# Optimization experiments

Measured on AMD Instinct MI355X. Metric: run time of the kernel, lower is better.

The kernel has to match this reference:

```python
import jax, jax.numpy as jnp
import numpy as np

PC_RANGE = (-51.2, -51.2, -5.0, 51.2, 51.2, 3.0)
NUM_HEADS = 8
K_TOKENS = 512
DS = 4  # bev_downsample


def _ln(x, w, b):
    m = x.mean(-1, keepdims=True)
    v = ((x - m) ** 2).mean(-1, keepdims=True)
    return (x - m) * jax.lax.rsqrt(v + 1e-5) * w + b


def _mlp(x, w1, b1, w2, b2):
    return jnp.maximum(x @ w1.T + b1, 0.0) @ w2.T + b2


def setup_inputs() -> dict:
    key = jax.random.key(0)
    ks = jax.random.split(key, 16)
    B, N, Dq, Dkv, H, W = 2, 1220, 512, 256, 512, 512
    s = 0.02
    rn = lambda k, shp: jax.random.normal(k, shp, jnp.float32) * s
    inp = {
        'instance_feature': jax.random.normal(ks[0], (B, N, Dq), jnp.float32),
        'pts_feats': jax.random.normal(ks[1], (B, Dkv, H, W), jnp.float32),
        'anchor': jax.random.normal(ks[2], (B, N, 11), jnp.float32) * 20.0,
        # cross-attention (kdim=vdim=256, embed_dim=512)
        'qw': rn(ks[3], (Dq, Dq)), 'qb': jnp.zeros((Dq,), jnp.float32),
        'kw': rn(ks[4], (Dq, Dkv)), 'kb': jnp.zeros((Dq,), jnp.float32),
        'vw': rn(ks[5], (Dq, Dkv)), 'vb': jnp.zeros((Dq,), jnp.float32),
        'aow': rn(ks[6], (Dq, Dq)), 'aob': jnp.zeros((Dq,), jnp.float32),
        # layer norms
        'qn_w': jnp.ones((Dq,), jnp.float32), 'qn_b': jnp.zeros((Dq,), jnp.float32),
        'tn_w': jnp.ones((Dkv,), jnp.float32), 'tn_b': jnp.zeros((Dkv,), jnp.float32),
        'on_w': jnp.ones((Dq,), jnp.float32), 'on_b': jnp.zeros((Dq,), jnp.float32),
        # out_proj
        'opw': rn(ks[7], (Dq, Dq)), 'opb': jnp.zeros((Dq,), jnp.float32),
        # bev_pos_mlp: Linear(2,256) -> ReLU -> Linear(256,256)
        'bp_w1': rn(ks[8], (Dkv, 2)), 'bp_b1': jnp.zeros((Dkv,), jnp.float32),
        'bp_w2': rn(ks[9], (Dkv, Dkv)), 'bp_b2': jnp.zeros((Dkv,), jnp.float32),
        # anchor_pos_mlp: Linear(2,512) -> ReLU -> Linear(512,512)
        'ap_w1': rn(ks[10], (Dq, 2)), 'ap_b1': jnp.zeros((Dq,), jnp.float32),
        'ap_w2': rn(ks[11], (Dq, Dq)), 'ap_b2': jnp.zeros((Dq,), jnp.float32),
        # gate: Linear(512,512) -> ReLU -> Linear(512,512) -> Sigmoid, bias init -2.0
        'g_w1': rn(ks[12], (Dq, Dq)), 'g_b1': jnp.zeros((Dq,), jnp.float32),
        'g_w2': rn(ks[13], (Dq, Dq)), 'g_b2': jnp.full((Dq,), -2.0, jnp.float32),
    }
    return inp


def reference(instance_feature, pts_feats, anchor,
              qw, qb, kw, kb, vw, vb, aow, aob,
              qn_w, qn_b, tn_w, tn_b, on_w, on_b,
              opw, opb,
              bp_w1, bp_b1, bp_w2, bp_b2,
              ap_w1, ap_b1, ap_w2, ap_b2,
              g_w1, g_b1, g_w2, g_b2):
    B, C, H0, W0 = pts_feats.shape
    # avg_pool2d(kernel=stride=DS)
    H, W = H0 // DS, W0 // DS
    bev = pts_feats.reshape(B, C, H, DS, W, DS).mean(axis=(3, 5))  # [B,C,H,W]
    # topk token selection by mean squared activation
    score = (bev ** 2).mean(axis=1).reshape(B, H * W)
    K = min(K_TOKENS, H * W)
    _, idx = jax.lax.top_k(score, K)  # [B,K], sorted descending
    tokens = bev.reshape(B, C, H * W).transpose(0, 2, 1)  # [B,HW,C]
    lidar_tokens = jnp.take_along_axis(tokens, idx[..., None], axis=1)  # [B,K,C]
    ys = idx // W
    xs = idx % W
    token_pos = jnp.stack([(xs.astype(jnp.float32) + 0.5) / W,
                           (ys.astype(jnp.float32) + 0.5) / H], axis=-1)  # [B,K,2]
    lidar_tokens = lidar_tokens + _mlp(token_pos, bp_w1, bp_b1, bp_w2, bp_b2)
    # anchor positional prior (anchor detached in original)
    xr = (anchor[..., 0] - PC_RANGE[0]) / (PC_RANGE[3] - PC_RANGE[0])
    yr = (anchor[..., 1] - PC_RANGE[1]) / (PC_RANGE[4] - PC_RANGE[1])
    xy = jnp.clip(jnp.stack([xr, yr], axis=-1), 0.0, 1.0)
    query_input = instance_feature + _mlp(xy, ap_w1, ap_b1, ap_w2, ap_b2)
    query = _ln(query_input, qn_w, qn_b)
    kv = _ln(lidar_tokens, tn_w, tn_b)
    # multihead cross-attention (dropout off / eval mode)
    Dq = query.shape[-1]
    hd = Dq // NUM_HEADS
    q = (query @ qw.T + qb).reshape(B, -1, NUM_HEADS, hd)  # [B,N,h,d]
    k = (kv @ kw.T + kb).reshape(B, K, NUM_HEADS, hd)      # [B,K,h,d]
    v = (kv @ vw.T + vb).reshape(B, K, NUM_HEADS, hd)
    scale = 1.0 / jnp.sqrt(jnp.float32(hd))
    att = jax.nn.softmax(jnp.einsum('bnhd,bkhd->bhnk', q, k) * scale, axis=-1)
    ctx = jnp.einsum('bhnk,bkhd->bnhd', att, v).reshape(B, -1, Dq)
    ctx = ctx @ aow.T + aob  # MHA out_proj
    lidar_context = _ln(ctx @ opw.T + opb, on_w, on_b)
    gate = jax.nn.sigmoid(_mlp(query_input, g_w1, g_b1, g_w2, g_b2))
    return instance_feature + gate * lidar_context
```

## Files before the change

### kernel.cpp

```cpp
#include <hip/hip_runtime.h>
#include <hip/hip_bf16.h>
#include <math.h>

constexpr int BB  = 2;
constexpr int NN  = 1220;
constexpr int DKV = 256;
constexpr int H0  = 512, W0 = 512;
constexpr int HH  = 128, WW = 128;
constexpr int HW  = HH * WW;
constexpr int KT  = 512;
constexpr int MR  = BB * NN;
constexpr int MPAD = 2496;

typedef __attribute__((ext_vector_type(8)))  short bf16x8;
typedef __attribute__((ext_vector_type(4)))  float f32x4;
typedef __attribute__((ext_vector_type(16))) float f32x16;

constexpr size_t B_BEV   = 0;
constexpr size_t B_SCORE = 67108864;
constexpr size_t B_IDX   = 67239936;
constexpr size_t B_WBF   = 67244032;
constexpr size_t B_KV    = 70914048;
constexpr size_t B_KG    = 71438336;
constexpr size_t B_VG    = 72486912;
constexpr size_t B_VT    = 73535488;
constexpr size_t B_H1    = 74584064;
constexpr size_t B_QI32  = 77139968;
constexpr size_t B_QI16  = 82251776;
constexpr size_t B_QUERY = 84807680;
constexpr size_t B_QG    = 87363584;
constexpr size_t B_CTX   = 89919488;
constexpr size_t B_AO    = 92475392;
constexpr size_t B_OPO   = 95031296;
constexpr size_t B_LC    = 100143104;
constexpr size_t B_G1    = 105254912;
constexpr size_t WS_NEED = 107810816;

constexpr size_t WO_QW = 0, WO_KW = 262144, WO_VW = 393216, WO_AOW = 524288,
                 WO_OPW = 786432, WO_APW2 = 1048576, WO_GW1 = 1310720, WO_GW2 = 1572864;

__device__ __forceinline__ void gload_lds16(void* lds, const void* g) {
  __builtin_amdgcn_global_load_lds((const __attribute__((address_space(1))) unsigned int*)g,
                                   (__attribute__((address_space(3))) unsigned int*)lds, 16, 0, 0);
}

__device__ __forceinline__ unsigned cvt_pk_bf16(float a, float b) {
  unsigned r;
  asm("v_cvt_pk_bf16_f32 %0, %1, %2" : "=v"(r) : "v"(a), "v"(b));
  return r;
}

__global__ __launch_bounds__(256) void wconv_kernel(
    const float* __restrict__ qw, const float* __restrict__ kw,
    const float* __restrict__ vw, const float* __restrict__ aow,
    const float* __restrict__ opw, const float* __restrict__ apw2,
    const float* __restrict__ gw1, const float* __restrict__ gw2,
    __hip_bfloat16* __restrict__ dst) {
  int i = blockIdx.x * 256 + threadIdx.x;
  const float* src; int off;
  if (i < 262144)       { src = qw;   off = 0; }
  else if (i < 393216)  { src = kw;   off = 262144; }
  else if (i < 524288)  { src = vw;   off = 393216; }
  else if (i < 786432)  { src = aow;  off = 524288; }
  else if (i < 1048576) { src = opw;  off = 786432; }
  else if (i < 1310720) { src = apw2; off = 1048576; }
  else if (i < 1572864) { src = gw1;  off = 1310720; }
  else                  { src = gw2;  off = 1572864; }
  dst[i] = __float2bfloat16(src[i - off]);
}

__global__ __launch_bounds__(256) void pool_kernel(const float* __restrict__ pts,
                                                   float* __restrict__ bev) {
  int o = blockIdx.x * 256 + threadIdx.x;
  int w  = o & (WW - 1);
  int h  = (o >> 7) & (HH - 1);
  int bc = o >> 14;
  const float* p = pts + ((bc * H0) + h * 4) * W0 + w * 4;
  float s = 0.f;
#pragma unroll
  for (int r = 0; r < 4; ++r) {
    float4 v = *(const float4*)(p + r * W0);
    s += v.x + v.y + v.z + v.w;
  }
  bev[o] = s * (1.f / 16.f);
}

__global__ __launch_bounds__(256) void score_kernel(const float* __restrict__ bev,
                                                    float* __restrict__ score) {
  int t = blockIdx.x * 256 + threadIdx.x;
  int b = t >> 14, p = t & (HW - 1);
  const float* base = bev + (size_t)(b * DKV) * HW + p;
  float acc = 0.f;
  for (int c = 0; c < DKV; ++c) {
    float v = base[c * HW];
    acc += v * v;
  }
  score[t] = acc * (1.f / DKV);
}

__global__ __launch_bounds__(1024) void topk_kernel(const float* __restrict__ score,
                                                    int* __restrict__ idx) {
  int b = blockIdx.x;
  const float* s = score + b * HW;
  __shared__ int hist[16][256];
  __shared__ int htot[256];
  __shared__ int sh_digit, sh_need, sh_cnt;
  int tid = threadIdx.x;
  int wv = tid >> 6;
  unsigned prefix = 0;
  int need = KT;
  for (int pass = 0; pass < 4; ++pass) {
    int shift = 24 - pass * 8;
    if (tid < 256) {
#pragma unroll
      for (int w = 0; w < 16; ++w) hist[w][tid] = 0;
    }
    __syncthreads();
    for (int p = tid; p < HW; p += 1024) {
      unsigned u = __float_as_uint(s[p]);
      bool match = (pass == 0) || ((u >> (shift + 8)) == prefix);
      if (match) atomicAdd(&hist[wv][(u >> shift) & 255], 1);
    }
    __syncthreads();
    if (tid < 256) {
      int t = 0;
#pragma unroll
      for (int w = 0; w < 16; ++w) t += hist[w][tid];
      htot[tid] = t;
    }
    __syncthreads();
    for (int off = 1; off < 256; off <<= 1) {
      int v = 0;
      if (tid < 256) v = htot[tid] + ((tid + off < 256) ? htot[tid + off] : 0);
      __syncthreads();
      if (tid < 256) htot[tid] = v;
      __syncthreads();
    }
    if (tid < 256) {
      int sfx = htot[tid], sfx1 = (tid < 255) ? htot[tid + 1] : 0;
      if (sfx >= need && sfx1 < need) { sh_digit = tid; sh_need = need - sfx1; }
    }
    __syncthreads();
    prefix = (prefix << 8) | (unsigned)sh_digit;
    need = sh_need;
    __syncthreads();
  }
  unsigned T = prefix;
  int r = need;
  if (tid == 0) sh_cnt = 0;
  __syncthreads();
  for (int p = tid; p < HW; p += 1024) {
    if (__float_as_uint(s[p]) > T) {
      int pos = atomicAdd(&sh_cnt, 1);
      idx[b * KT + pos] = p;
    }
  }
  __syncthreads();
  int base = sh_cnt;
  if (tid < 64) {
    int taken = 0;
    for (int c0 = 0; c0 < HW && taken < r; c0 += 64) {
      int p = c0 + tid;
      bool eq = (__float_as_uint(s[p]) == T);
      unsigned long long m = __ballot(eq);
      int rank = __popcll(m & ((1ull << tid) - 1ull));
      if (eq && (taken + rank) < r) idx[b * KT + base + taken + rank] = p;
      taken += __popcll(m);
    }
  }
}

__global__ __launch_bounds__(256) void token_kernel(const float* __restrict__ bev,
    const int* __restrict__ idx,
    const float* __restrict__ bw1, const float* __restrict__ bb1,
    const float* __restrict__ bw2, const float* __restrict__ bb2,
    const float* __restrict__ tw, const float* __restrict__ tb,
    __hip_bfloat16* __restrict__ kv) {
  int blk = blockIdx.x;
  int b = blk >> 9;
  int c = threadIdx.x;
  int p = idx[blk];
  float val = bev[(size_t)(b * DKV + c) * HW + p];
  float px = ((p & (WW - 1)) + 0.5f) * (1.f / WW);
  float py = ((p >> 7) + 0.5f) * (1.f / HH);
  __shared__ float h1[DKV];
  __shared__ float red[DKV];
  h1[c] = fmaxf(bw1[c * 2] * px + bw1[c * 2 + 1] * py + bb1[c], 0.f);
  __syncthreads();
  float o = bb2[c];
  const float4* w4 = (const float4*)(bw2 + c * DKV);
#pragma unroll 4
  for (int j = 0; j < DKV / 4; ++j) {
    float4 w = w4[j];
    o += w.x * h1[j * 4] + w.y * h1[j * 4 + 1] + w.z * h1[j * 4 + 2] + w.w * h1[j * 4 + 3];
  }
  float tokv = val + o;
  red[c] = tokv; __syncthreads();
  for (int st = 128; st > 0; st >>= 1) { if (c < st) red[c] += red[c + st]; __syncthreads(); }
  float mean = red[0] * (1.f / DKV);
  __syncthreads();
  float d = tokv - mean;
  red[c] = d * d; __syncthreads();
  for (int st = 128; st > 0; st >>= 1) { if (c < st) red[c] += red[c + st]; __syncthreads(); }
  float inv = rsqrtf(red[0] * (1.f / DKV) + 1e-5f);
  kv[(size_t)blk * DKV + c] = __float2bfloat16(d * inv * tw[c] + tb[c]);
}

__global__ __launch_bounds__(256) void ap1_kernel(const float* __restrict__ anchor,
    const float* __restrict__ w1, const float* __restrict__ b1,
    __hip_bfloat16* __restrict__ h) {
  int g = blockIdx.x * 256 + threadIdx.x;
  int row = g >> 9, col = g & 511;
  float ax = anchor[row * 11 + 0];
  float ay = anchor[row * 11 + 1];
  float xr = fminf(fmaxf((ax + 51.2f) * (1.f / 102.4f), 0.f), 1.f);
  float yr = fminf(fmaxf((ay + 51.2f) * (1.f / 102.4f), 0.f), 1.f);
  h[g] = __float2bfloat16(fmaxf(w1[col * 2] * xr + w1[col * 2 + 1] * yr + b1[col], 0.f));
}

template <int EPI>
__global__ __launch_bounds__(256) void mgemm(
    const short* __restrict__ A, const short* __restrict__ W,
    const float* __restrict__ bias, const float* __restrict__ aux1,
    const float* __restrict__ aux2, void* __restrict__ o1, void* __restrict__ o2,
    int M, int Nd, int Kd) {
  __shared__ short As[64 * 64];
  __shared__ short Bs[64 * 64];
  const int tid = threadIdx.x;
  const int wave = tid >> 6, lane = tid & 63;
  const int m0 = blockIdx.y * 64, n0 = blockIdx.x * 64;
  const int wr = wave >> 1, wc = wave & 1;
  f32x4 acc[2][2];
#pragma unroll
  for (int i = 0; i < 2; ++i)
#pragma unroll
    for (int j = 0; j < 2; ++j) acc[i][j] = (f32x4){0.f, 0.f, 0.f, 0.f};

  const int srow = lane >> 3;
  const int sslot = lane & 7;
  for (int k0 = 0; k0 < Kd; k0 += 64) {
#pragma unroll
    for (int half = 0; half < 2; ++half) {
      int r = wave * 16 + half * 8 + srow;
      int ss = sslot ^ (r & 7);
      gload_lds16(As + (wave * 16 + half * 8) * 64,
                  A + (size_t)(m0 + r) * Kd + k0 + ss * 8);
      gload_lds16(Bs + (wave * 16 + half * 8) * 64,
                  W + (size_t)(n0 + r) * Kd + k0 + ss * 8);
    }
    __syncthreads();
#pragma unroll
    for (int ks = 0; ks < 2; ++ks) {
      bf16x8 af[2], bf[2];
#pragma unroll
      for (int mf = 0; mf < 2; ++mf) {
        int r = wr * 32 + mf * 16 + (lane & 15);
        int slot = (ks * 4 + (lane >> 4)) ^ (r & 7);
        af[mf] = *(const bf16x8*)(As + r * 64 + slot * 8);
      }
#pragma unroll
      for (int nf = 0; nf < 2; ++nf) {
        int r = wc * 32 + nf * 16 + (lane & 15);
        int slot = (ks * 4 + (lane >> 4)) ^ (r & 7);
        bf[nf] = *(const bf16x8*)(Bs + r * 64 + slot * 8);
      }
#pragma unroll
      for (int mf = 0; mf < 2; ++mf)
#pragma unroll
        for (int nf = 0; nf < 2; ++nf)
          acc[mf][nf] = __builtin_amdgcn_mfma_f32_16x16x32_bf16(af[mf], bf[nf], acc[mf][nf], 0, 0, 0);
    }
    __syncthreads();
  }
#pragma unroll
  for (int mf = 0; mf < 2; ++mf)
#pragma unroll
    for (int nf = 0; nf < 2; ++nf) {
      int col = n0 + wc * 32 + nf * 16 + (lane & 15);
      float bv = bias[col];
#pragma unroll
      for (int i = 0; i < 4; ++i) {
        int row = m0 + wr * 32 + mf * 16 + (lane >> 4) * 4 + i;
        if (row < M) {
          float v = acc[mf][nf][i] + bv;
          size_t off = (size_t)row * Nd + col;
          if (EPI == 0) ((__hip_bfloat16*)o1)[off] = __float2bfloat16(v);
          else if (EPI == 1) {
            v += aux1[off];
            ((float*)o1)[off] = v;
            ((__hip_bfloat16*)o2)[off] = __float2bfloat16(v);
          } else if (EPI == 2) ((__hip_bfloat16*)o1)[off] = __float2bfloat16(fmaxf(v, 0.f));
          else if (EPI == 3) ((__hip_bfloat16*)o1)[off] = __float2bfloat16(v * 0.125f);
          else if (EPI == 4) ((float*)o1)[off] = v;
          else if (EPI == 5) {
            float g = 1.f / (1.f + __expf(-v));
            ((float*)o1)[off] = aux1[off] + g * aux2[off];
          }
        }
      }
    }
}

template <int OUT_BF16>
__global__ __launch_bounds__(256) void ln512_kernel(const float* __restrict__ in,
    void* __restrict__ outp, const float* __restrict__ w, const float* __restrict__ bb) {
  int row = blockIdx.x, tid = threadIdx.x;
  float x0 = in[(size_t)row * 512 + tid];
  float x1 = in[(size_t)row * 512 + 256 + tid];
  __shared__ float rs[256], rq[256];
  rs[tid] = x0 + x1;
  rq[tid] = x0 * x0 + x1 * x1;
  __syncthreads();
  for (int o = 128; o > 0; o >>= 1) {
    if (tid < o) { rs[tid] += rs[tid + o]; rq[tid] += rq[tid + o]; }
    __syncthreads();
  }
  float mean = rs[0] * (1.f / 512.f);
  float var = rq[0] * (1.f / 512.f) - mean * mean;
  float inv = rsqrtf(var + 1e-5f);
  float y0 = (x0 - mean) * inv * w[tid] + bb[tid];
  float y1 = (x1 - mean) * inv * w[256 + tid] + bb[256 + tid];
  if (OUT_BF16) {
    ((__hip_bfloat16*)outp)[(size_t)row * 512 + tid] = __float2bfloat16(y0);
    ((__hip_bfloat16*)outp)[(size_t)row * 512 + 256 + tid] = __float2bfloat16(y1);
  } else {
    ((float*)outp)[(size_t)row * 512 + tid] = y0;
    ((float*)outp)[(size_t)row * 512 + 256 + tid] = y1;
  }
}

__global__ __launch_bounds__(256) void vtrans_kernel(const short* __restrict__ V,
                                                     short* __restrict__ Vt) {
  __shared__ short tile[128][72];
  int tc = blockIdx.x, h = blockIdx.y, b = blockIdx.z;
  int tid = threadIdx.x;
#pragma unroll
  for (int it = 0; it < 8; ++it) {
    int e = it * 256 + tid;
    int r = e >> 4, c = (e & 15) * 4;
    *(short4*)&tile[r][c] =
        *(const short4*)(V + ((size_t)(b * 512 + tc * 128 + r)) * 512 + h * 64 + c);
  }
  __syncthreads();
#pragma unroll
  for (int it = 0; it < 8; ++it) {
    int e = it * 256 + tid;
    int d = e >> 5, t4 = (e & 31) * 4;
    short4 v;
    v.x = tile[t4 + 0][d]; v.y = tile[t4 + 1][d];
    v.z = tile[t4 + 2][d]; v.w = tile[t4 + 3][d];
    *(short4*)(Vt + (((size_t)(b * 8 + h)) * 64 + d) * 512 + tc * 128 + t4) = v;
  }
}

__global__ __launch_bounds__(256) void attn_kernel(
    const short* __restrict__ Qg, const short* __restrict__ Kg,
    const short* __restrict__ Vt, __hip_bfloat16* __restrict__ ctx) {
  int tid = threadIdx.x;
  int wid = blockIdx.x * 4 + (tid >> 6);
  int lane = tid & 63;
  int l31 = lane & 31, lhi = lane >> 5;
  int qc = wid % 39;
  int bh = wid / 39;
  int h = bh & 7, b = bh >> 3;
  int n = qc * 32 + l31;
  size_t qrow = (size_t)b * NN + n;
  const short* qp = Qg + qrow * 512 + h * 64 + lhi * 8;
  bf16x8 qf0 = *(const bf16x8*)(qp);
  bf16x8 qf1 = *(const bf16x8*)(qp + 16);
  bf16x8 qf2 = *(const bf16x8*)(qp + 32);
  bf16x8 qf3 = *(const bf16x8*)(qp + 48);
  f32x16 ot0 = {}, ot1 = {};
  float m_run = -1e30f, lsum = 0.f;
  const short* kbase = Kg + ((size_t)(b * KT) + l31) * 512 + h * 64 + lhi * 8;
  const short* vbase = Vt + (((size_t)(b * 8 + h)) * 64 + l31) * 512 + lhi * 8;
  for (int tc = 0; tc < 16; ++tc) {
    const short* kp = kbase + (size_t)(tc * 32) * 512;
    bf16x8 kf0 = *(const bf16x8*)(kp);
    bf16x8 kf1 = *(const bf16x8*)(kp + 16);
    bf16x8 kf2 = *(const bf16x8*)(kp + 32);
    bf16x8 kf3 = *(const bf16x8*)(kp + 48);
    const short* vp = vbase + tc * 32;
    bf16x8 v00 = *(const bf16x8*)(vp);
    bf16x8 v01 = *(const bf16x8*)(vp + 16);
    bf16x8 v10 = *(const bf16x8*)(vp + 32 * 512);
    bf16x8 v11 = *(const bf16x8*)(vp + 32 * 512 + 16);
    f32x16 s = {};
    s = __builtin_amdgcn_mfma_f32_32x32x16_bf16(kf0, qf0, s, 0, 0, 0);
    s = __builtin_amdgcn_mfma_f32_32x32x16_bf16(kf1, qf1, s, 0, 0, 0);
    s = __builtin_amdgcn_mfma_f32_32x32x16_bf16(kf2, qf2, s, 0, 0, 0);
    s = __builtin_amdgcn_mfma_f32_32x32x16_bf16(kf3, qf3, s, 0, 0, 0);
    float pmax = s[0];
#pragma unroll
    for (int i = 1; i < 16; ++i) pmax = fmaxf(pmax, s[i]);
    pmax = fmaxf(pmax, __shfl_xor(pmax, 32));
    float m_new = fmaxf(m_run, pmax);
    float corr = __expf(m_run - m_new);
    m_run = m_new;
    lsum *= corr;
#pragma unroll
    for (int i = 0; i < 16; ++i) { ot0[i] *= corr; ot1[i] *= corr; }
    float p[16];
    float psum = 0.f;
#pragma unroll
    for (int i = 0; i < 16; ++i) { p[i] = __expf(s[i] - m_new); psum += p[i]; }
    lsum += psum;
    unsigned w0 = cvt_pk_bf16(p[0], p[1]),  w1 = cvt_pk_bf16(p[2], p[3]);
    unsigned w2 = cvt_pk_bf16(p[4], p[5]),  w3 = cvt_pk_bf16(p[6], p[7]);
    unsigned w4 = cvt_pk_bf16(p[8], p[9]),  w5 = cvt_pk_bf16(p[10], p[11]);
    unsigned w6 = cvt_pk_bf16(p[12], p[13]), w7 = cvt_pk_bf16(p[14], p[15]);
    unsigned sw0 = (unsigned)__shfl_xor((int)w0, 32), sw1 = (unsigned)__shfl_xor((int)w1, 32);
    unsigned sw2 = (unsigned)__shfl_xor((int)w2, 32), sw3 = (unsigned)__shfl_xor((int)w3, 32);
    unsigned sw4 = (unsigned)__shfl_xor((int)w4, 32), sw5 = (unsigned)__shfl_xor((int)w5, 32);
    unsigned sw6 = (unsigned)__shfl_xor((int)w6, 32), sw7 = (unsigned)__shfl_xor((int)w7, 32);
    union UU { unsigned u[4]; bf16x8 v; };
    UU ub0, ub1;
    ub0.u[0] = lhi ? sw2 : w0; ub0.u[1] = lhi ? sw3 : w1;
    ub0.u[2] = lhi ? w2 : sw0; ub0.u[3] = lhi ? w3 : sw1;
    ub1.u[0] = lhi ? sw6 : w4; ub1.u[1] = lhi ? sw7 : w5;
    ub1.u[2] = lhi ? w6 : sw4; ub1.u[3] = lhi ? w7 : sw5;
    ot0 = __builtin_amdgcn_mfma_f32_32x32x16_bf16(v00, ub0.v, ot0, 0, 0, 0);
    ot0 = __builtin_amdgcn_mfma_f32_32x32x16_bf16(v01, ub1.v, ot0, 0, 0, 0);
    ot1 = __builtin_amdgcn_mfma_f32_32x32x16_bf16(v10, ub0.v, ot1, 0, 0, 0);
    ot1 = __builtin_amdgcn_mfma_f32_32x32x16_bf16(v11, ub1.v, ot1, 0, 0, 0);
  }
  lsum += __shfl_xor(lsum, 32);
  float inv = 1.f / lsum;
  if (n < NN) {
    __hip_bfloat16* cp = ctx + qrow * 512 + h * 64;
#pragma unroll
    for (int r = 0; r < 16; ++r) {
      int d = (r & 3) + 8 * (r >> 2) + 4 * lhi;
      cp[d]      = __float2bfloat16(ot0[r] * inv);
      cp[32 + d] = __float2bfloat16(ot1[r] * inv);
    }
  }
}

extern "C" void kernel_launch(void* const* d_in, const int* in_sizes, int n_in,
                              void* d_out, int out_size, void* d_ws, size_t ws_size,
                              hipStream_t stream) {
  const float* inst   = (const float*)d_in[0];
  const float* pts    = (const float*)d_in[1];
  const float* anchor = (const float*)d_in[2];
  const float* qw  = (const float*)d_in[3];
  const float* qb  = (const float*)d_in[4];
  const float* kw  = (const float*)d_in[5];
  const float* kb  = (const float*)d_in[6];
  const float* vw  = (const float*)d_in[7];
  const float* vb  = (const float*)d_in[8];
  const float* aow = (const float*)d_in[9];
  const float* aob = (const float*)d_in[10];
  const float* qnw = (const float*)d_in[11];
  const float* qnb = (const float*)d_in[12];
  const float* tnw = (const float*)d_in[13];
  const float* tnb = (const float*)d_in[14];
  const float* onw = (const float*)d_in[15];
  const float* onb = (const float*)d_in[16];
  const float* opw = (const float*)d_in[17];
  const float* opb = (const float*)d_in[18];
  const float* bpw1 = (const float*)d_in[19];
  const float* bpb1 = (const float*)d_in[20];
  const float* bpw2 = (const float*)d_in[21];
  const float* bpb2 = (const float*)d_in[22];
  const float* apw1 = (const float*)d_in[23];
  const float* apb1 = (const float*)d_in[24];
  const float* apw2 = (const float*)d_in[25];
  const float* apb2 = (const float*)d_in[26];
  const float* gw1 = (const float*)d_in[27];
  const float* gb1 = (const float*)d_in[28];
  const float* gw2 = (const float*)d_in[29];
  const float* gb2 = (const float*)d_in[30];
  float* out = (float*)d_out;

  if (ws_size < WS_NEED) return;
  char* ws = (char*)d_ws;
  float* bev   = (float*)(ws + B_BEV);
  float* score = (float*)(ws + B_SCORE);
  int*   idx   = (int*)(ws + B_IDX);
  short* wbf   = (short*)(ws + B_WBF);
  __hip_bfloat16* kvb = (__hip_bfloat16*)(ws + B_KV);
  short* Kgb  = (short*)(ws + B_KG);
  short* Vgb  = (short*)(ws + B_VG);
  short* Vtb  = (short*)(ws + B_VT);
  short* h1b  = (short*)(ws + B_H1);
  float* qi32 = (float*)(ws + B_QI32);
  short* qi16 = (short*)(ws + B_QI16);
  short* qryb = (short*)(ws + B_QUERY);
  short* Qgb  = (short*)(ws + B_QG);
  short* ctxb = (short*)(ws + B_CTX);
  short* aobuf = (short*)(ws + B_AO);
  float* opo  = (float*)(ws + B_OPO);
  float* lc   = (float*)(ws + B_LC);
  short* g1b  = (short*)(ws + B_G1);

  wconv_kernel<<<7168, 256, 0, stream>>>(qw, kw, vw, aow, opw, apw2, gw1, gw2,
                                         (__hip_bfloat16*)wbf);
  pool_kernel<<<BB * DKV * HW / 256, 256, 0, stream>>>(pts, bev);
  score_kernel<<<BB * HW / 256, 256, 0, stream>>>(bev, score);
  topk_kernel<<<BB, 1024, 0, stream>>>(score, idx);
  token_kernel<<<BB * KT, 256, 0, stream>>>(bev, idx, bpw1, bpb1, bpw2, bpb2, tnw, tnb, kvb);
  mgemm<0><<<dim3(8, 16), 256, 0, stream>>>((const short*)kvb, wbf + WO_KW, kb,
                                            nullptr, nullptr, Kgb, nullptr, 1024, 512, 256);
  mgemm<0><<<dim3(8, 16), 256, 0, stream>>>((const short*)kvb, wbf + WO_VW, vb,
                                            nullptr, nullptr, Vgb, nullptr, 1024, 512, 256);
  vtrans_kernel<<<dim3(4, 8, BB), 256, 0, stream>>>(Vgb, Vtb);
  ap1_kernel<<<MR * 512 / 256, 256, 0, stream>>>(anchor, apw1, apb1, (__hip_bfloat16*)h1b);
  mgemm<1><<<dim3(8, 39), 256, 0, stream>>>(h1b, wbf + WO_APW2, apb2, inst, nullptr,
                                            qi32, qi16, MR, 512, 512);
  ln512_kernel<1><<<MR, 256, 0, stream>>>(qi32, qryb, qnw, qnb);
  mgemm<3><<<dim3(8, 39), 256, 0, stream>>>(qryb, wbf + WO_QW, qb, nullptr, nullptr,
                                            Qgb, nullptr, MR, 512, 512);
  attn_kernel<<<156, 256, 0, stream>>>(Qgb, Kgb, Vtb, (__hip_bfloat16*)ctxb);
  mgemm<0><<<dim3(8, 39), 256, 0, stream>>>(ctxb, wbf + WO_AOW, aob, nullptr, nullptr,
                                            aobuf, nullptr, MR, 512, 512);
  mgemm<4><<<dim3(8, 39), 256, 0, stream>>>(aobuf, wbf + WO_OPW, opb, nullptr, nullptr,
                                            opo, nullptr, MR, 512, 512);
  ln512_kernel<0><<<MR, 256, 0, stream>>>(opo, lc, onw, onb);
  mgemm<2><<<dim3(8, 39), 256, 0, stream>>>(qi16, wbf + WO_GW1, gb1, nullptr, nullptr,
                                            g1b, nullptr, MR, 512, 512);
  mgemm<5><<<dim3(8, 39), 256, 0, stream>>>(g1b, wbf + WO_GW2, gb2, inst, lc,
                                            out, nullptr, MR, 512, 512);
}
```

Baseline: 357.1 us.

## Use 128x64 double-buffered LDS tiles in mgemm and shrink workspace layout

Result: slower. 381.3 us (+6.8%).

```diff
diff --git a/kernel.cpp b/kernel.cpp
--- a/kernel.cpp
+++ b/kernel.cpp
@@ -10,31 +10,31 @@
 constexpr int HW  = HH * WW;
 constexpr int KT  = 512;
 constexpr int MR  = BB * NN;
-constexpr int MPAD = 2496;
+constexpr int MPAD = 2560;
 
 typedef __attribute__((ext_vector_type(8)))  short bf16x8;
 typedef __attribute__((ext_vector_type(4)))  float f32x4;
 typedef __attribute__((ext_vector_type(16))) float f32x16;
 
 constexpr size_t B_BEV   = 0;
-constexpr size_t B_SCORE = 67108864;
-constexpr size_t B_IDX   = 67239936;
-constexpr size_t B_WBF   = 67244032;
-constexpr size_t B_KV    = 70914048;
-constexpr size_t B_KG    = 71438336;
-constexpr size_t B_VG    = 72486912;
-constexpr size_t B_VT    = 73535488;
-constexpr size_t B_H1    = 74584064;
-constexpr size_t B_QI32  = 77139968;
-constexpr size_t B_QI16  = 82251776;
-constexpr size_t B_QUERY = 84807680;
-constexpr size_t B_QG    = 87363584;
-constexpr size_t B_CTX   = 89919488;
-constexpr size_t B_AO    = 92475392;
-constexpr size_t B_OPO   = 95031296;
-constexpr size_t B_LC    = 100143104;
-constexpr size_t B_G1    = 105254912;
-constexpr size_t WS_NEED = 107810816;
+constexpr size_t B_SCORE = 33554432;
+constexpr size_t B_IDX   = 33685504;
+constexpr size_t B_WBF   = 33689600;
+constexpr size_t B_KV    = 37359616;
+constexpr size_t B_KG    = 37883904;
+constexpr size_t B_VG    = 38932480;
+constexpr size_t B_VT    = 39981056;
+constexpr size_t B_H1    = 41029632;
+constexpr size_t B_QI32  = 43651072;
+constexpr size_t B_QI16  = 48893952;
+constexpr size_t B_QUERY = 51515392;
+constexpr size_t B_QG    = 54136832;
+constexpr size_t B_CTX   = 56758272;
+constexpr size_t B_AO    = 59379712;
+constexpr size_t B_OPO   = 62001152;
+constexpr size_t B_LC    = 67244032;
+constexpr size_t B_G1    = 72486912;
+constexpr size_t WS_NEED = 75112448;
 
 constexpr size_t WO_QW = 0, WO_KW = 262144, WO_VW = 393216, WO_AOW = 524288,
                  WO_OPW = 786432, WO_APW2 = 1048576, WO_GW1 = 1310720, WO_GW2 = 1572864;
@@ -180,7 +180,7 @@
   int b = blk >> 9;
   int c = threadIdx.x;
   int p = idx[blk];
-  float val = bev[(size_t)(b * DKV + c) * HW + p];
+  float val = bev[((size_t)(b * DKV + c) << 14) + p];
   float px = ((p & (WW - 1)) + 0.5f) * (1.f / WW);
   float py = ((p >> 7) + 0.5f) * (1.f / HH);
   __shared__ float h1[DKV];
@@ -224,63 +224,76 @@
     const float* __restrict__ bias, const float* __restrict__ aux1,
     const float* __restrict__ aux2, void* __restrict__ o1, void* __restrict__ o2,
     int M, int Nd, int Kd) {
-  __shared__ short As[64 * 64];
-  __shared__ short Bs[64 * 64];
+  __shared__ short As[2][128 * 64];
+  __shared__ short Bs[2][64 * 64];
   const int tid = threadIdx.x;
   const int wave = tid >> 6, lane = tid & 63;
-  const int m0 = blockIdx.y * 64, n0 = blockIdx.x * 64;
-  const int wr = wave >> 1, wc = wave & 1;
-  f32x4 acc[2][2];
+  const int m0 = blockIdx.y * 128, n0 = blockIdx.x * 64;
+  const int srow = lane >> 3, sslot = lane & 7;
+  const int ss = sslot ^ srow;
+  f32x4 acc[2][4];
 #pragma unroll
   for (int i = 0; i < 2; ++i)
 #pragma unroll
-    for (int j = 0; j < 2; ++j) acc[i][j] = (f32x4){0.f, 0.f, 0.f, 0.f};
-
-  const int srow = lane >> 3;
-  const int sslot = lane & 7;
-  for (int k0 = 0; k0 < Kd; k0 += 64) {
-#pragma unroll
-    for (int half = 0; half < 2; ++half) {
-      int r = wave * 16 + half * 8 + srow;
-      int ss = sslot ^ (r & 7);
-      gload_lds16(As + (wave * 16 + half * 8) * 64,
-                  A + (size_t)(m0 + r) * Kd + k0 + ss * 8);
-      gload_lds16(Bs + (wave * 16 + half * 8) * 64,
-                  W + (size_t)(n0 + r) * Kd + k0 + ss * 8);
-    }
-    __syncthreads();
+    for (int j = 0; j < 4; ++j) acc[i][j] = (f32x4){0.f, 0.f, 0.f, 0.f};
+
+  const short* Abase = A + (size_t)(m0 + srow) * Kd + ss * 8;
+  const short* Wbase = W + (size_t)(n0 + srow) * Kd + ss * 8;
+  const int nk = Kd >> 6;
+
+#define STAGE(buf, k0)                                                        \
+  {                                                                           \
+    _Pragma("unroll")                                                         \
+    for (int u = 0; u < 4; ++u) {                                             \
+      int unit = wave * 4 + u;                                                \
+      gload_lds16(&As[buf][unit * 512], Abase + (size_t)(unit * 8) * Kd + (k0)); \
+    }                                                                         \
+    _Pragma("unroll")                                                         \
+    for (int u = 0; u < 2; ++u) {                                             \
+      int unit = wave * 2 + u;                                                \
+      gload_lds16(&Bs[buf][unit * 512], Wbase + (size_t)(unit * 8) * Kd + (k0)); \
+    }                                                                         \
+  }
+
+  STAGE(0, 0);
+  __syncthreads();
+  for (int t = 0; t < nk; ++t) {
+    if (t + 1 < nk) STAGE((t + 1) & 1, (t + 1) << 6);
+    const short* as = As[t & 1];
+    const short* bs = Bs[t & 1];
 #pragma unroll
     for (int ks = 0; ks < 2; ++ks) {
-      bf16x8 af[2], bf[2];
+      bf16x8 af[2], bf[4];
 #pragma unroll
       for (int mf = 0; mf < 2; ++mf) {
-        int r = wr * 32 + mf * 16 + (lane & 15);
-        int slot = (ks * 4 + (lane >> 4)) ^ (r & 7);
-        af[mf] = *(const bf16x8*)(As + r * 64 + slot * 8);
+        int rr = wave * 32 + mf * 16 + (lane & 15);
+        int slot = (ks * 4 + (lane >> 4)) ^ (rr & 7);
+        af[mf] = *(const bf16x8*)(as + rr * 64 + slot * 8);
       }
 #pragma unroll
-      for (int nf = 0; nf < 2; ++nf) {
-        int r = wc * 32 + nf * 16 + (lane & 15);
-        int slot = (ks * 4 + (lane >> 4)) ^ (r & 7);
-        bf[nf] = *(const bf16x8*)(Bs + r * 64 + slot * 8);
+      for (int nf = 0; nf < 4; ++nf) {
+        int rr = nf * 16 + (lane & 15);
+        int slot = (ks * 4 + (lane >> 4)) ^ (rr & 7);
+        bf[nf] = *(const bf16x8*)(bs + rr * 64 + slot * 8);
       }
 #pragma unroll
       for (int mf = 0; mf < 2; ++mf)
 #pragma unroll
-        for (int nf = 0; nf < 2; ++nf)
+        for (int nf = 0; nf < 4; ++nf)
           acc[mf][nf] = __builtin_amdgcn_mfma_f32_16x16x32_bf16(af[mf], bf[nf], acc[mf][nf], 0, 0, 0);
     }
     __syncthreads();
   }
+#undef STAGE
 #pragma unroll
   for (int mf = 0; mf < 2; ++mf)
 #pragma unroll
-    for (int nf = 0; nf < 2; ++nf) {
-      int col = n0 + wc * 32 + nf * 16 + (lane & 15);
+    for (int nf = 0; nf < 4; ++nf) {
+      int col = n0 + nf * 16 + (lane & 15);
       float bv = bias[col];
 #pragma unroll
       for (int i = 0; i < 4; ++i) {
-        int row = m0 + wr * 32 + mf * 16 + (lane >> 4) * 4 + i;
+        int row = m0 + wave * 32 + mf * 16 + (lane >> 4) * 4 + i;
         if (row < M) {
           float v = acc[mf][nf][i] + bv;
           size_t off = (size_t)row * Nd + col;
@@ -405,9 +418,9 @@
 #pragma unroll
     for (int i = 0; i < 16; ++i) { p[i] = __expf(s[i] - m_new); psum += p[i]; }
     lsum += psum;
-    unsigned w0 = cvt_pk_bf16(p[0], p[1]),  w1 = cvt_pk_bf16(p[2], p[3]);
-    unsigned w2 = cvt_pk_bf16(p[4], p[5]),  w3 = cvt_pk_bf16(p[6], p[7]);
-    unsigned w4 = cvt_pk_bf16(p[8], p[9]),  w5 = cvt_pk_bf16(p[10], p[11]);
+    unsigned w0 = cvt_pk_bf16(p[0], p[1]),   w1 = cvt_pk_bf16(p[2], p[3]);
+    unsigned w2 = cvt_pk_bf16(p[4], p[5]),   w3 = cvt_pk_bf16(p[6], p[7]);
+    unsigned w4 = cvt_pk_bf16(p[8], p[9]),   w5 = cvt_pk_bf16(p[10], p[11]);
     unsigned w6 = cvt_pk_bf16(p[12], p[13]), w7 = cvt_pk_bf16(p[14], p[15]);
     unsigned sw0 = (unsigned)__shfl_xor((int)w0, 32), sw1 = (unsigned)__shfl_xor((int)w1, 32);
     unsigned sw2 = (unsigned)__shfl_xor((int)w2, 32), sw3 = (unsigned)__shfl_xor((int)w3, 32);
@@ -500,25 +513,25 @@
   score_kernel<<<BB * HW / 256, 256, 0, stream>>>(bev, score);
   topk_kernel<<<BB, 1024, 0, stream>>>(score, idx);
   token_kernel<<<BB * KT, 256, 0, stream>>>(bev, idx, bpw1, bpb1, bpw2, bpb2, tnw, tnb, kvb);
-  mgemm<0><<<dim3(8, 16), 256, 0, stream>>>((const short*)kvb, wbf + WO_KW, kb,
-                                            nullptr, nullptr, Kgb, nullptr, 1024, 512, 256);
-  mgemm<0><<<dim3(8, 16), 256, 0, stream>>>((const short*)kvb, wbf + WO_VW, vb,
-                                            nullptr, nullptr, Vgb, nullptr, 1024, 512, 256);
+  mgemm<0><<<dim3(8, 8), 256, 0, stream>>>((const short*)kvb, wbf + WO_KW, kb,
+                                           nullptr, nullptr, Kgb, nullptr, 1024, 512, 256);
+  mgemm<0><<<dim3(8, 8), 256, 0, stream>>>((const short*)kvb, wbf + WO_VW, vb,
+                                           nullptr, nullptr, Vgb, nullptr, 1024, 512, 256);
   vtrans_kernel<<<dim3(4, 8, BB), 256, 0, stream>>>(Vgb, Vtb);
   ap1_kernel<<<MR * 512 / 256, 256, 0, stream>>>(anchor, apw1, apb1, (__hip_bfloat16*)h1b);
-  mgemm<1><<<dim3(8, 39), 256, 0, stream>>>(h1b, wbf + WO_APW2, apb2, inst, nullptr,
+  mgemm<1><<<dim3(8, 20), 256, 0, stream>>>(h1b, wbf + WO_APW2, apb2, inst, nullptr,
                                             qi32, qi16, MR, 512, 512);
   ln512_kernel<1><<<MR, 256, 0, stream>>>(qi32, qryb, qnw, qnb);
-  mgemm<3><<<dim3(8, 39), 256, 0, stream>>>(qryb, wbf + WO_QW, qb, nullptr, nullptr,
+  mgemm<3><<<dim3(8, 20), 256, 0, stream>>>(qryb, wbf + WO_QW, qb, nullptr, nullptr,
                                             Qgb, nullptr, MR, 512, 512);
   attn_kernel<<<156, 256, 0, stream>>>(Qgb, Kgb, Vtb, (__hip_bfloat16*)ctxb);
-  mgemm<0><<<dim3(8, 39), 256, 0, stream>>>(ctxb, wbf + WO_AOW, aob, nullptr, nullptr,
+  mgemm<0><<<dim3(8, 20), 256, 0, stream>>>(ctxb, wbf + WO_AOW, aob, nullptr, nullptr,
                                             aobuf, nullptr, MR, 512, 512);
-  mgemm<4><<<dim3(8, 39), 256, 0, stream>>>(aobuf, wbf + WO_OPW, opb, nullptr, nullptr,
+  mgemm<4><<<dim3(8, 20), 256, 0, stream>>>(aobuf, wbf + WO_OPW, opb, nullptr, nullptr,
                                             opo, nullptr, MR, 512, 512);
   ln512_kernel<0><<<MR, 256, 0, stream>>>(opo, lc, onw, onb);
-  mgemm<2><<<dim3(8, 39), 256, 0, stream>>>(qi16, wbf + WO_GW1, gb1, nullptr, nullptr,
+  mgemm<2><<<dim3(8, 20), 256, 0, stream>>>(qi16, wbf + WO_GW1, gb1, nullptr, nullptr,
                                             g1b, nullptr, MR, 512, 512);
-  mgemm<5><<<dim3(8, 39), 256, 0, stream>>>(g1b, wbf + WO_GW2, gb2, inst, lc,
+  mgemm<5><<<dim3(8, 20), 256, 0, stream>>>(g1b, wbf + WO_GW2, gb2, inst, lc,
                                             out, nullptr, MR, 512, 512);
 }
```
